# Kernel optimization log

Hardware: AMD Instinct MI355X
Metric: run time of the kernel (lower is better)

The kernel has to match this reference:

```python
import jax, jax.numpy as jnp
import numpy as np

HIDDEN_DIM = 2048
NUM_CONN = int(HIDDEN_DIM * HIDDEN_DIM * 0.1)  # 419430


def setup_inputs() -> dict:
    key = jax.random.key(0)
    k1, k2, k3 = jax.random.split(key, 3)
    x = jax.random.normal(k1, (4, 2048, HIDDEN_DIM), dtype=jnp.float32)
    connection_indices = jax.random.randint(k2, (2, NUM_CONN), 0, HIDDEN_DIM, dtype=jnp.int64)
    connection_values = jax.random.normal(k3, (NUM_CONN,), dtype=jnp.float32) * 0.001
    alpha = jnp.asarray(0.01, dtype=jnp.float32)
    return {"x": x, "connection_indices": connection_indices,
            "connection_values": connection_values, "alpha": alpha}


def reference(x, connection_indices, connection_values, alpha):
    # Rebuild dense W from COO (duplicate indices sum, matching sparse_coo_tensor.to_dense())
    H = x.shape[-1]
    W = jnp.zeros((H, H), dtype=x.dtype).at[connection_indices[0], connection_indices[1]].add(connection_values)
    # torch.matmul(x, W.T): out[b,s,i] = sum_j x[b,s,j] * W[i,j]
    lateral = jnp.einsum('bsj,ij->bsi', x, W)
    return x + alpha * lateral
```

## Files before the change

kernel.cpp:

```cpp
#include <hip/hip_runtime.h>


typedef unsigned short u16;
typedef __attribute__((ext_vector_type(8))) short bf16x8;
typedef __attribute__((ext_vector_type(4))) float f32x4;

#define HID 2048
#define BM 128
#define BN 256
#define BK 32
#define NT (HID / BK)
#define ASZ (BM * BK)
#define BSZ (BN * BK)
#define SLOT (ASZ + BSZ)

__device__ __forceinline__ u16 f2bf(float f) {
    unsigned u = __builtin_bit_cast(unsigned, f);
    u += 0x7fffu + ((u >> 16) & 1u);
    return (u16)(u >> 16);
}

__device__ __forceinline__ void cvt8(const float* __restrict__ src,
                                     u16* __restrict__ dst, int i) {
    const float4* p = (const float4*)src + (size_t)i * 2;
    float4 a = p[0], b = p[1];
    uint4 o;
    o.x = (unsigned)f2bf(a.x) | ((unsigned)f2bf(a.y) << 16);
    o.y = (unsigned)f2bf(a.z) | ((unsigned)f2bf(a.w) << 16);
    o.z = (unsigned)f2bf(b.x) | ((unsigned)f2bf(b.y) << 16);
    o.w = (unsigned)f2bf(b.z) | ((unsigned)f2bf(b.w) << 16);
    ((uint4*)dst)[i] = o;
}

__global__ void cvt_f32_bf16_kernel(const float* __restrict__ in,
                                    u16* __restrict__ out, int n8) {
    int stride = gridDim.x * blockDim.x;
    for (int i = blockIdx.x * blockDim.x + threadIdx.x; i < n8; i += stride)
        cvt8(in, out, i);
}

__global__ void scatter_coo_kernel(const int* __restrict__ idx,
                                   const float* __restrict__ vals,
                                   float* __restrict__ W, int nnz) {
    int n = blockIdx.x * blockDim.x + threadIdx.x;
    if (n < nnz)
        atomicAdd(W + (size_t)idx[n] * HID + idx[nnz + n], vals[n]);
}

__global__ void prep_kernel(const int* __restrict__ idx,
                            const float* __restrict__ vals,
                            float* __restrict__ W, int nnz,
                            const float* __restrict__ x,
                            u16* __restrict__ xb, int n8x) {
    int gid = blockIdx.x * blockDim.x + threadIdx.x;
    if (gid < nnz)
        atomicAdd(W + (size_t)idx[gid] * HID + idx[nnz + gid], vals[gid]);
    int stride = gridDim.x * blockDim.x;
    for (int i = gid; i < n8x; i += stride)
        cvt8(x, xb, i);
}

#define GLDS(gsrc, ldst)                                                   \
    __builtin_amdgcn_global_load_lds(                                      \
        (const __attribute__((address_space(1))) void*)(gsrc),             \
        (__attribute__((address_space(3))) void*)(ldst), 16, 0, 0)

__global__ __launch_bounds__(512, 4) void gemm3_kernel(
        const u16* __restrict__ A,
        const u16* __restrict__ B,
        const float* __restrict__ alphap,
        float* __restrict__ out) {
    __shared__ u16 lds[3 * SLOT];

    const int t = threadIdx.x;
    const int lane = t & 63;
    const int w = t >> 6;
    const int wr = w >> 2;
    const int wc = w & 3;
    const int fr = lane & 15;
    const int kg = lane >> 4;

    const int bid = blockIdx.x;
    const int swz = (bid & 7) * 64 + (bid >> 3);
    const int bm = swz >> 3;
    const int bn = swz & 7;
    const size_t rowBase = (size_t)bm * BM;
    const size_t colBase = (size_t)bn * BN;

    const int srowA = (w << 4) + (lane >> 2);
    const int sgA = (lane & 3) ^ ((srowA >> 1) & 3);
    const u16* aSrc = A + (rowBase + srowA) * HID + sgA * 8;
    const int adst = w * 512 + lane * 8;

    const int srowB = (w << 5) + (lane >> 2);
    const int sgB = (lane & 3) ^ ((srowB >> 1) & 3);
    const u16* bSrc0 = B + (colBase + srowB) * HID + sgB * 8;
    const u16* bSrc1 = bSrc0 + (size_t)16 * HID;
    const int bdst0 = ASZ + w * 1024 + lane * 8;
    const int bdst1 = bdst0 + 512;

    const int gread = kg ^ ((fr >> 1) & 3);
    const int aRdOff = (wr * 64 + fr) * BK + gread * 8;
    const int bRdOff = ASZ + (wc * 64 + fr) * BK + gread * 8;

    f32x4 acc[4][4] = {};

#pragma unroll
    for (int pt = 0; pt < 2; ++pt) {
        u16* s = lds + pt * SLOT;
        GLDS(aSrc + pt * BK, s + adst);
        GLDS(bSrc0 + pt * BK, s + bdst0);
        GLDS(bSrc1 + pt * BK, s + bdst1);
    }
    asm volatile("s_waitcnt vmcnt(3)" ::: "memory");
    __builtin_amdgcn_s_barrier();
    __builtin_amdgcn_sched_barrier(0);

    int cur = 0;
#pragma unroll 1
    for (int tt = 0; tt < NT; ++tt) {
        u16* slot = lds + cur * SLOT;
        const int wIdx = cur + 2 >= 3 ? cur - 1 : cur + 2;
        u16* slotW = lds + wIdx * SLOT;

        bf16x8 a[4], b[4];
#pragma unroll
        for (int m = 0; m < 4; ++m)
            a[m] = *(const bf16x8*)(slot + aRdOff + m * 512);
#pragma unroll
        for (int n = 0; n < 4; ++n)
            b[n] = *(const bf16x8*)(slot + bRdOff + n * 512);

        if (tt + 2 < NT) {
            const int koff = (tt + 2) * BK;
            GLDS(aSrc + koff, slotW + adst);
            GLDS(bSrc0 + koff, slotW + bdst0);
            GLDS(bSrc1 + koff, slotW + bdst1);
        }

        asm volatile("s_waitcnt lgkmcnt(0)" ::: "memory");
        __builtin_amdgcn_sched_barrier(0);
        if (tt <= NT - 3)      asm volatile("s_waitcnt vmcnt(3)" ::: "memory");
        else if (tt == NT - 2) asm volatile("s_waitcnt vmcnt(0)" ::: "memory");
        __builtin_amdgcn_s_barrier();
        __builtin_amdgcn_sched_barrier(0);

        __builtin_amdgcn_s_setprio(1);
#pragma unroll
        for (int m = 0; m < 4; ++m)
#pragma unroll
            for (int n = 0; n < 4; ++n)
                acc[m][n] = __builtin_amdgcn_mfma_f32_16x16x32_bf16(
                    a[m], b[n], acc[m][n], 0, 0, 0);
        __builtin_amdgcn_s_setprio(0);

        cur = cur == 2 ? 0 : cur + 1;
    }

    const float alphav = *alphap;
#pragma unroll
    for (int m = 0; m < 4; ++m) {
#pragma unroll
        for (int n = 0; n < 4; ++n) {
            f32x4 c = acc[m][n];
            const size_t gn = colBase + wc * 64 + n * 16 + fr;
#pragma unroll
            for (int j = 0; j < 4; ++j) {
                const size_t gm = rowBase + wr * 64 + m * 16 + kg * 4 + j;
                const size_t o = gm * HID + gn;
                unsigned xu = ((unsigned)A[o]) << 16;
                float xf = __builtin_bit_cast(float, xu);
                __builtin_nontemporal_store(xf + alphav * c[j], &out[o]);
            }
        }
    }
}

extern "C" void kernel_launch(void* const* d_in, const int* in_sizes, int n_in,
                              void* d_out, int out_size, void* d_ws, size_t ws_size,
                              hipStream_t stream) {
    const float* x     = (const float*)d_in[0];
    const int*   idx   = (const int*)d_in[1];
    const float* vals  = (const float*)d_in[2];
    const float* alpha = (const float*)d_in[3];
    float* out = (float*)d_out;

    const int nnz = in_sizes[2];
    const size_t MB = 1024 * 1024;
    const int n8W = (HID * HID) / 8;
    const int n8X = in_sizes[0] / 8;
    const int grid = (8192 / BM) * (HID / BN);

    if (ws_size >= 56 * MB) {
        u16*   Xb = (u16*)d_ws;
        u16*   Wb = (u16*)((char*)d_ws + 32 * MB);
        float* Wf = (float*)((char*)d_ws + 40 * MB);
        hipMemsetAsync(Wf, 0, (size_t)HID * HID * sizeof(float), stream);
        prep_kernel<<<2048, 256, 0, stream>>>(idx, vals, Wf, nnz, x, Xb, n8X);
        cvt_f32_bf16_kernel<<<2048, 256, 0, stream>>>(Wf, Wb, n8W);
        gemm3_kernel<<<grid, 512, 0, stream>>>(Xb, Wb, alpha, out);
    } else {
        float* Wf = (float*)d_ws;
        u16*   Xb = (u16*)d_ws;
        u16*   Wb = (u16*)((char*)d_ws + 32 * MB);
        hipMemsetAsync(Wf, 0, (size_t)HID * HID * sizeof(float), stream);
        scatter_coo_kernel<<<(nnz + 255) / 256, 256, 0, stream>>>(idx, vals, Wf, nnz);
        cvt_f32_bf16_kernel<<<2048, 256, 0, stream>>>(Wf, Wb, n8W);
        cvt_f32_bf16_kernel<<<2048, 256, 0, stream>>>(x, Xb, n8X);
        gemm3_kernel<<<grid, 512, 0, stream>>>(Xb, Wb, alpha, out);
    }
}
```

Before: 211.4 us.

## Enlarge GEMM tile to 256x256x64 with 8-phase double-buffered LDS pipeline

Replaces the 128x256x32 triple-buffered GEMM with a 256x256 tile and BK=64. Each K step is split into four MFMA phases, and the next tile's A and B quarter loads are interleaved between those phases using double-buffered 128KB LDS. Each wave now holds 8x4 accumulators. The larger tile raises arithmetic intensity and halves the number of global tile loads per output. The cost is lower occupancy (launch bounds 2), more barriers per iteration, and a grid of 256 blocks. The epilogue also switches from nontemporal stores to plain stores.

```diff
diff --git a/kernel.cpp b/kernel.cpp
--- a/kernel.cpp
+++ b/kernel.cpp
@@ -6,13 +6,11 @@
 typedef __attribute__((ext_vector_type(4))) float f32x4;
 
 #define HID 2048
-#define BM 128
+#define BM 256
 #define BN 256
-#define BK 32
+#define BK 64
 #define NT (HID / BK)
-#define ASZ (BM * BK)
-#define BSZ (BN * BK)
-#define SLOT (ASZ + BSZ)
+#define QSZ 8192
 
 __device__ __forceinline__ u16 f2bf(float f) {
     unsigned u = __builtin_bit_cast(unsigned, f);
@@ -65,115 +63,151 @@
         (const __attribute__((address_space(1))) void*)(gsrc),             \
         (__attribute__((address_space(3))) void*)(ldst), 16, 0, 0)
 
-__global__ __launch_bounds__(512, 4) void gemm3_kernel(
+#define BAR()   __builtin_amdgcn_s_barrier()
+#define SBAR()  __builtin_amdgcn_sched_barrier(0)
+#define LGKM0() asm volatile("s_waitcnt lgkmcnt(0)" ::: "memory")
+
+__global__ __launch_bounds__(512, 2) void gemm8p_kernel(
         const u16* __restrict__ A,
         const u16* __restrict__ B,
         const float* __restrict__ alphap,
         float* __restrict__ out) {
-    __shared__ u16 lds[3 * SLOT];
-
-    const int t = threadIdx.x;
-    const int lane = t & 63;
-    const int w = t >> 6;
+    __shared__ u16 sh[8 * QSZ];
+
+    const int tid = threadIdx.x;
+    const int lane = tid & 63;
+    const int w = tid >> 6;
     const int wr = w >> 2;
     const int wc = w & 3;
     const int fr = lane & 15;
     const int kg = lane >> 4;
+    const int xr = lane & 7;
 
     const int bid = blockIdx.x;
-    const int swz = (bid & 7) * 64 + (bid >> 3);
-    const int bm = swz >> 3;
-    const int bn = swz & 7;
+    const int swz = (bid & 7) * 32 + (bid >> 3);
+    const int bm = swz & 31;
+    const int bn = swz >> 5;
     const size_t rowBase = (size_t)bm * BM;
     const size_t colBase = (size_t)bn * BN;
 
-    const int srowA = (w << 4) + (lane >> 2);
-    const int sgA = (lane & 3) ^ ((srowA >> 1) & 3);
-    const u16* aSrc = A + (rowBase + srowA) * HID + sgA * 8;
-    const int adst = w * 512 + lane * 8;
-
-    const int srowB = (w << 5) + (lane >> 2);
-    const int sgB = (lane & 3) ^ ((srowB >> 1) & 3);
-    const u16* bSrc0 = B + (colBase + srowB) * HID + sgB * 8;
-    const u16* bSrc1 = bSrc0 + (size_t)16 * HID;
-    const int bdst0 = ASZ + w * 1024 + lane * 8;
-    const int bdst1 = bdst0 + 512;
-
-    const int gread = kg ^ ((fr >> 1) & 3);
-    const int aRdOff = (wr * 64 + fr) * BK + gread * 8;
-    const int bRdOff = ASZ + (wc * 64 + fr) * BK + gread * 8;
-
-    f32x4 acc[4][4] = {};
-
-#pragma unroll
-    for (int pt = 0; pt < 2; ++pt) {
-        u16* s = lds + pt * SLOT;
-        GLDS(aSrc + pt * BK, s + adst);
-        GLDS(bSrc0 + pt * BK, s + bdst0);
-        GLDS(bSrc1 + pt * BK, s + bdst1);
+    const int tb = tid >> 3;
+    const int g8 = ((tid & 7) ^ (tb & 7)) << 3;
+    const u16* aS = A + (rowBase + tb) * HID + g8;
+    const u16* bS = B + (colBase + tb) * HID + g8;
+    const int dst8 = tid * 8;
+
+#define ST_A(buf, qa, tt) do {                                             \
+    GLDS(aS + ((qa) * 128) * HID + (tt) * BK,                              \
+         sh + (((buf) << 2) | (qa)) * QSZ + dst8);                         \
+    GLDS(aS + ((qa) * 128 + 64) * HID + (tt) * BK,                         \
+         sh + (((buf) << 2) | (qa)) * QSZ + 4096 + dst8);                  \
+} while (0)
+#define ST_B(buf, h, tt) do {                                              \
+    GLDS(bS + ((h) * 128) * HID + (tt) * BK,                               \
+         sh + (((buf) << 2) | (2 + (h))) * QSZ + dst8);                    \
+    GLDS(bS + ((h) * 128 + 64) * HID + (tt) * BK,                          \
+         sh + (((buf) << 2) | (2 + (h))) * QSZ + 4096 + dst8);             \
+} while (0)
+
+    const int gk0 = ((kg ^ xr)) << 3;
+    const int gk1 = (((4 | kg) ^ xr)) << 3;
+
+    f32x4 acc[8][4] = {};
+
+    ST_B(0, 0, 0); ST_B(0, 1, 0);
+    ST_A(0, 0, 0); ST_A(0, 1, 0);
+    ST_B(1, 0, 1); ST_B(1, 1, 1);
+    asm volatile("s_waitcnt vmcnt(4)" ::: "memory");
+    BAR(); SBAR();
+
+#pragma unroll 1
+    for (int t = 0; t < NT; ++t) {
+        const int bufR = t & 1, bufW = bufR ^ 1;
+        const u16* aq = sh + (((bufR << 2) | wr) * QSZ) + fr * 64;
+        const u16* bq = sh + (((bufR << 2) | 2 | (wc >> 1)) * QSZ)
+                           + ((wc & 1) << 12) + fr * 64;
+        bf16x8 av[4], bv[4];
+
+#pragma unroll
+        for (int m = 0; m < 4; ++m) av[m] = *(const bf16x8*)(aq + m * 1024 + gk0);
+#pragma unroll
+        for (int n = 0; n < 4; ++n) bv[n] = *(const bf16x8*)(bq + n * 1024 + gk0);
+        if (t + 1 < NT) ST_A(bufW, 0, t + 1);
+        BAR(); LGKM0(); SBAR();
+        __builtin_amdgcn_s_setprio(1);
+#pragma unroll
+        for (int m = 0; m < 4; ++m)
+#pragma unroll
+            for (int n = 0; n < 4; ++n)
+                acc[m][n] = __builtin_amdgcn_mfma_f32_16x16x32_bf16(
+                    av[m], bv[n], acc[m][n], 0, 0, 0);
+        __builtin_amdgcn_s_setprio(0);
+        BAR(); SBAR();
+
+#pragma unroll
+        for (int m = 0; m < 4; ++m) av[m] = *(const bf16x8*)(aq + (m + 4) * 1024 + gk0);
+        if (t + 1 < NT) ST_A(bufW, 1, t + 1);
+        BAR(); LGKM0(); SBAR();
+        __builtin_amdgcn_s_setprio(1);
+#pragma unroll
+        for (int m = 0; m < 4; ++m)
+#pragma unroll
+            for (int n = 0; n < 4; ++n)
+                acc[m + 4][n] = __builtin_amdgcn_mfma_f32_16x16x32_bf16(
+                    av[m], bv[n], acc[m + 4][n], 0, 0, 0);
+        __builtin_amdgcn_s_setprio(0);
+        BAR(); SBAR();
+
+#pragma unroll
+        for (int m = 0; m < 4; ++m) av[m] = *(const bf16x8*)(aq + m * 1024 + gk1);
+#pragma unroll
+        for (int n = 0; n < 4; ++n) bv[n] = *(const bf16x8*)(bq + n * 1024 + gk1);
+        BAR(); LGKM0(); SBAR();
+        __builtin_amdgcn_s_setprio(1);
+#pragma unroll
+        for (int m = 0; m < 4; ++m)
+#pragma unroll
+            for (int n = 0; n < 4; ++n)
+                acc[m][n] = __builtin_amdgcn_mfma_f32_16x16x32_bf16(
+                    av[m], bv[n], acc[m][n], 0, 0, 0);
+        __builtin_amdgcn_s_setprio(0);
+        BAR(); SBAR();
+
+#pragma unroll
+        for (int m = 0; m < 4; ++m) av[m] = *(const bf16x8*)(aq + (m + 4) * 1024 + gk1);
+        if (t + 2 < NT) { ST_B(bufR, 0, t + 2); ST_B(bufR, 1, t + 2); }
+        BAR(); LGKM0(); SBAR();
+        __builtin_amdgcn_s_setprio(1);
+#pragma unroll
+        for (int m = 0; m < 4; ++m)
+#pragma unroll
+            for (int n = 0; n < 4; ++n)
+                acc[m + 4][n] = __builtin_amdgcn_mfma_f32_16x16x32_bf16(
+                    av[m], bv[n], acc[m + 4][n], 0, 0, 0);
+        __builtin_amdgcn_s_setprio(0);
+        if (t + 2 < NT)      asm volatile("s_waitcnt vmcnt(4)" ::: "memory");
+        else if (t + 1 < NT) asm volatile("s_waitcnt vmcnt(0)" ::: "memory");
+        BAR(); SBAR();
     }
-    asm volatile("s_waitcnt vmcnt(3)" ::: "memory");
-    __builtin_amdgcn_s_barrier();
-    __builtin_amdgcn_sched_barrier(0);
-
-    int cur = 0;
-#pragma unroll 1
-    for (int tt = 0; tt < NT; ++tt) {
-        u16* slot = lds + cur * SLOT;
-        const int wIdx = cur + 2 >= 3 ? cur - 1 : cur + 2;
-        u16* slotW = lds + wIdx * SLOT;
-
-        bf16x8 a[4], b[4];
-#pragma unroll
-        for (int m = 0; m < 4; ++m)
-            a[m] = *(const bf16x8*)(slot + aRdOff + m * 512);
-#pragma unroll
-        for (int n = 0; n < 4; ++n)
-            b[n] = *(const bf16x8*)(slot + bRdOff + n * 512);
-
-        if (tt + 2 < NT) {
-            const int koff = (tt + 2) * BK;
-            GLDS(aSrc + koff, slotW + adst);
-            GLDS(bSrc0 + koff, slotW + bdst0);
-            GLDS(bSrc1 + koff, slotW + bdst1);
-        }
-
-        asm volatile("s_waitcnt lgkmcnt(0)" ::: "memory");
-        __builtin_amdgcn_sched_barrier(0);
-        if (tt <= NT - 3)      asm volatile("s_waitcnt vmcnt(3)" ::: "memory");
-        else if (tt == NT - 2) asm volatile("s_waitcnt vmcnt(0)" ::: "memory");
-        __builtin_amdgcn_s_barrier();
-        __builtin_amdgcn_sched_barrier(0);
-
-        __builtin_amdgcn_s_setprio(1);
-#pragma unroll
-        for (int m = 0; m < 4; ++m)
-#pragma unroll
-            for (int n = 0; n < 4; ++n)
-                acc[m][n] = __builtin_amdgcn_mfma_f32_16x16x32_bf16(
-                    a[m], b[n], acc[m][n], 0, 0, 0);
-        __builtin_amdgcn_s_setprio(0);
-
-        cur = cur == 2 ? 0 : cur + 1;
-    }
 
     const float alphav = *alphap;
 #pragma unroll
-    for (int m = 0; m < 4; ++m) {
+    for (int m = 0; m < 8; ++m) {
 #pragma unroll
         for (int n = 0; n < 4; ++n) {
             f32x4 c = acc[m][n];
             const size_t gn = colBase + wc * 64 + n * 16 + fr;
 #pragma unroll
             for (int j = 0; j < 4; ++j) {
-                const size_t gm = rowBase + wr * 64 + m * 16 + kg * 4 + j;
+                const size_t gm = rowBase + wr * 128 + m * 16 + kg * 4 + j;
                 const size_t o = gm * HID + gn;
                 unsigned xu = ((unsigned)A[o]) << 16;
-                float xf = __builtin_bit_cast(float, xu);
-                __builtin_nontemporal_store(xf + alphav * c[j], &out[o]);
+                out[o] = __builtin_bit_cast(float, xu) + alphav * c[j];
             }
         }
     }
+#undef ST_A
+#undef ST_B
 }
 
 extern "C" void kernel_launch(void* const* d_in, const int* in_sizes, int n_in,
@@ -198,7 +232,7 @@
         hipMemsetAsync(Wf, 0, (size_t)HID * HID * sizeof(float), stream);
         prep_kernel<<<2048, 256, 0, stream>>>(idx, vals, Wf, nnz, x, Xb, n8X);
         cvt_f32_bf16_kernel<<<2048, 256, 0, stream>>>(Wf, Wb, n8W);
-        gemm3_kernel<<<grid, 512, 0, stream>>>(Xb, Wb, alpha, out);
+        gemm8p_kernel<<<grid, 512, 0, stream>>>(Xb, Wb, alpha, out);
     } else {
         float* Wf = (float*)d_ws;
         u16*   Xb = (u16*)d_ws;
@@ -207,6 +241,6 @@
         scatter_coo_kernel<<<(nnz + 255) / 256, 256, 0, stream>>>(idx, vals, Wf, nnz);
         cvt_f32_bf16_kernel<<<2048, 256, 0, stream>>>(Wf, Wb, n8W);
         cvt_f32_bf16_kernel<<<2048, 256, 0, stream>>>(x, Xb, n8X);
-        gemm3_kernel<<<grid, 512, 0, stream>>>(Xb, Wb, alpha, out);
+        gemm8p_kernel<<<grid, 512, 0, stream>>>(Xb, Wb, alpha, out);
     }
 }
```

Result: no change. 212.5 us (+0.5%).
